# Kernel optimization log

Hardware: AMD Instinct MI355X
Metric: run time of the kernel (lower is better)

Reference implementation:

```python
import jax, jax.numpy as jnp
import numpy as np

N, T, D, H = 256, 128, 512, 1024


def setup_inputs() -> dict:
    key = jax.random.key(0)
    k_x, k_A, k_Wx, k_Wh, k_Wa = jax.random.split(key, 5)
    x = jax.random.normal(k_x, (N, T, D), dtype=jnp.float32)
    A = jax.random.normal(k_A, (N, H, 4, 4), dtype=jnp.float32)
    Wx = jax.random.normal(k_Wx, (D, 4 * H), dtype=jnp.float32) / np.sqrt(D)
    Wh = jax.random.normal(k_Wh, (H, 4 * H), dtype=jnp.float32) / np.sqrt(H)
    Wattn = jax.random.normal(k_Wa, (H, 4 * H), dtype=jnp.float32) / np.sqrt(H)
    b = jnp.zeros((4 * H,), dtype=jnp.float32)
    return {"x": x, "A": A, "Wx": Wx, "Wh": Wh, "Wattn": Wattn, "b": b}


def _attention_lstm(x, A, Wx, Wh, Wattn, b):
    # A: (N, H, 4, 4) -> flatten spatial to (N, H, 16)
    A_flat = A.reshape(A.shape[0], A.shape[1], -1)
    h0 = A_flat.mean(axis=2)  # (N, H)
    c0 = h0
    Hdim = h0.shape[1]
    scale = 1.0 / jnp.sqrt(jnp.asarray(Hdim, dtype=x.dtype))

    def step(carry, x_t):
        prev_h, prev_c = carry
        # scaled dot-product attention over 16 spatial locations
        scores = jnp.einsum("nh,nhs->ns", prev_h, A_flat) * scale  # (N, 16)
        w = jax.nn.softmax(scores, axis=1)
        attn = jnp.einsum("nhs,ns->nh", A_flat, w)  # (N, H)
        # fused LSTM gates
        a = x_t @ Wx + prev_h @ Wh + attn @ Wattn + b  # (N, 4H)
        i = jax.nn.sigmoid(a[:, 0:Hdim])
        f = jax.nn.sigmoid(a[:, Hdim:2 * Hdim])
        o = jax.nn.sigmoid(a[:, 2 * Hdim:3 * Hdim])
        g = jnp.tanh(a[:, 3 * Hdim:4 * Hdim])
        next_c = f * prev_c + i * g
        next_h = o * jnp.tanh(next_c)
        return (next_h, next_c), next_h

    x_tnd = jnp.swapaxes(x, 0, 1)  # (T, N, D)
    _, h_tnh = jax.lax.scan(step, (h0, c0), x_tnd)
    return jnp.swapaxes(h_tnh, 0, 1)  # (N, T, H)


def reference(x, A, Wx, Wh, Wattn, b):
    return _attention_lstm(x, A, Wx, Wh, Wattn, b)
```

## Files before the change

kernel.cpp:

```cpp
#include <hip/hip_runtime.h>
#include <math.h>

#define NB 256
#define TT 128
#define DD 512
#define HH 1024
#define KHX 1536
#define KFB 2560
#define BK 128
#define NBLK4 256

typedef _Float16 half_t;
typedef _Float16 half8 __attribute__((ext_vector_type(8)));
typedef _Float16 half4v __attribute__((ext_vector_type(4)));
typedef _Float16 half2v __attribute__((ext_vector_type(2)));
typedef float f32x4 __attribute__((ext_vector_type(4)));


__global__ __launch_bounds__(256) void k_trans(const float* __restrict__ src,
        half_t* __restrict__ dst, int kstride, int koff, int nkt) {
    __shared__ half_t tile[64][65];
    int bk = blockIdx.x % nkt;
    int bn = blockIdx.x / nkt;
    int k0 = bk * 64, n0 = bn * 64;
    #pragma unroll
    for (int i = 0; i < 16; ++i) {
        int idx = i * 256 + threadIdx.x;
        int r = idx >> 6, c = idx & 63;
        tile[c][r] = (half_t)src[(size_t)(k0 + r) * 4096 + n0 + c];
    }
    __syncthreads();
    #pragma unroll
    for (int i = 0; i < 16; ++i) {
        int idx = i * 256 + threadIdx.x;
        int r = idx >> 6, c = idx & 63;
        dst[(size_t)(n0 + r) * kstride + koff + k0 + c] = tile[r][c];
    }
}

__global__ __launch_bounds__(256) void k_convX(const float* __restrict__ x,
        half_t* __restrict__ x16) {
    size_t base = ((size_t)blockIdx.x * 256 + threadIdx.x) * 32;
    #pragma unroll
    for (int u = 0; u < 4; ++u) {
        float4 a = ((const float4*)(x + base))[2 * u];
        float4 c = ((const float4*)(x + base))[2 * u + 1];
        half8 p;
        p[0] = (half_t)a.x; p[1] = (half_t)a.y; p[2] = (half_t)a.z; p[3] = (half_t)a.w;
        p[4] = (half_t)c.x; p[5] = (half_t)c.y; p[6] = (half_t)c.z; p[7] = (half_t)c.w;
        ((half8*)(x16 + base))[u] = p;
    }
}

__global__ __launch_bounds__(256) void k_convA2(const float* __restrict__ A,
        half_t* __restrict__ A16, half_t* __restrict__ AsT,
        float* __restrict__ cbuf, half_t* __restrict__ h16) {
    int n = blockIdx.x, tid = threadIdx.x;
    #pragma unroll
    for (int r = 0; r < 4; ++r) {
        int h = tid + r * 256;
        const float4* ap = (const float4*)(A + ((size_t)n * HH + h) * 16);
        float4 v0 = ap[0], v1 = ap[1], v2 = ap[2], v3 = ap[3];
        float a[16];
        a[0]=v0.x; a[1]=v0.y; a[2] =v0.z; a[3] =v0.w;
        a[4]=v1.x; a[5]=v1.y; a[6] =v1.z; a[7] =v1.w;
        a[8]=v2.x; a[9]=v2.y; a[10]=v2.z; a[11]=v2.w;
        a[12]=v3.x; a[13]=v3.y; a[14]=v3.z; a[15]=v3.w;
        float hv = 0.f;
        #pragma unroll
        for (int s = 0; s < 16; ++s) hv += a[s];
        hv *= (1.f / 16.f);
        size_t ci = (size_t)n * HH + h;
        cbuf[ci] = hv;
        h16[ci] = (half_t)hv;
        half8 q0, q1;
        #pragma unroll
        for (int s = 0; s < 8; ++s) { q0[s] = (half_t)a[s]; q1[s] = (half_t)a[s + 8]; }
        *(half8*)(A16 + ci * 16) = q0;
        *(half8*)(A16 + ci * 16 + 8) = q1;
        #pragma unroll
        for (int s = 0; s < 16; ++s)
            AsT[(size_t)n * 16 * HH + (size_t)s * HH + h] = (half_t)a[s];
    }
}

__global__ __launch_bounds__(256) void k_initsc(const half_t* __restrict__ h16,
        const half_t* __restrict__ A16,
        float* __restrict__ sc0, float* __restrict__ sc1, float* __restrict__ sc2) {
    __shared__ float sred[4][16];
    int n = blockIdx.x, tid = threadIdx.x;
    float ps[16];
    #pragma unroll
    for (int s = 0; s < 16; ++s) ps[s] = 0.f;
    #pragma unroll
    for (int r = 0; r < 4; ++r) {
        int h = tid + r * 256;
        size_t ci = (size_t)n * HH + h;
        float hv = (float)h16[ci];
        const half8* ap = (const half8*)(A16 + ci * 16);
        half8 a0 = ap[0], a1 = ap[1];
        #pragma unroll
        for (int s = 0; s < 8; ++s) {
            ps[s]     += hv * (float)a0[s];
            ps[s + 8] += hv * (float)a1[s];
        }
    }
    #pragma unroll
    for (int off = 32; off; off >>= 1)
        #pragma unroll
        for (int s = 0; s < 16; ++s) ps[s] += __shfl_xor(ps[s], off, 64);
    int wave = tid >> 6;
    if ((tid & 63) == 0)
        #pragma unroll
        for (int s = 0; s < 16; ++s) sred[wave][s] = ps[s];
    __syncthreads();
    if (tid < 16)
        sc0[(size_t)n * 16 + tid] =
            sred[0][tid] + sred[1][tid] + sred[2][tid] + sred[3][tid];
    if (tid < 112) {
        int x = 1 + tid / 16, s = tid % 16;
        sc0[((size_t)x * 256 + n) * 16 + s] = 0.f;
    }
    if (tid < 128) {
        int x = tid / 16, s = tid % 16;
        sc1[((size_t)x * 256 + n) * 16 + s] = 0.f;
        sc2[((size_t)x * 256 + n) * 16 + s] = 0.f;
    }
}

__global__ __launch_bounds__(256) void k_gemm_G(const half_t* __restrict__ AsT,
        const half_t* __restrict__ WaT, half_t* __restrict__ G16) {
    __shared__ half_t sAs[16][BK + 8];
    __shared__ half_t sB[4][16][BK + 8];
    int bid = blockIdx.x;
    int n = bid >> 6, jt = bid & 63;
    int j0 = jt * 16;
    int tid = threadIdx.x, wv = tid >> 6, lane = tid & 63;
    f32x4 acc = {};
    int srB = tid >> 2, scB = (tid & 3) * 32;
    int gB = srB >> 4, jcB = srB & 15;
    for (int it = 0; it < HH / BK; ++it) {
        int k0 = it * BK;
        if (tid < 128) {
            int r = tid >> 3, c = (tid & 7) * 16;
            const uint4* sp = (const uint4*)(AsT + (size_t)n * 16 * HH + (size_t)r * HH + k0 + c);
            uint4 u0 = sp[0], u1 = sp[1];
            *(uint4*)&sAs[r][c] = u0;
            *(uint4*)&sAs[r][c + 8] = u1;
        }
        {
            const half_t* src = WaT + ((size_t)(gB * HH + j0 + jcB)) * HH + k0 + scB;
            uint4 u0 = ((const uint4*)src)[0];
            uint4 u1 = ((const uint4*)src)[1];
            uint4 u2 = ((const uint4*)src)[2];
            uint4 u3 = ((const uint4*)src)[3];
            *((uint4*)&sB[gB][jcB][scB])      = u0;
            *((uint4*)&sB[gB][jcB][scB + 8])  = u1;
            *((uint4*)&sB[gB][jcB][scB + 16]) = u2;
            *((uint4*)&sB[gB][jcB][scB + 24]) = u3;
        }
        __syncthreads();
        int row16 = lane & 15, kg = lane >> 4;
        #pragma unroll
        for (int kc = 0; kc < BK / 32; ++kc) {
            half8 bf = *(const half8*)&sB[wv][row16][kc * 32 + kg * 8];
            half8 af = *(const half8*)&sAs[row16][kc * 32 + kg * 8];
            acc = __builtin_amdgcn_mfma_f32_16x16x32_f16(af, bf, acc, 0, 0, 0);
        }
        __syncthreads();
    }
    int col = lane & 15, rbase = (lane >> 4) * 4;
    size_t jf = (size_t)wv * HH + j0 + col;
    half4v o;
    o[0] = (half_t)acc[0]; o[1] = (half_t)acc[1];
    o[2] = (half_t)acc[2]; o[3] = (half_t)acc[3];
    *(half4v*)(G16 + ((size_t)n * 4096 + jf) * 16 + rbase) = o;
}

__global__ __launch_bounds__(256) void k_gemm_XW(const half_t* __restrict__ x16,
        const half_t* __restrict__ WhxT, half_t* __restrict__ XW16) {
    __shared__ half_t sA[128][72];
    __shared__ half_t sB[64][72];
    int bid = blockIdx.x;
    int bm = bid & 255;
    int bj = bid >> 8;
    int row0 = bm * 128;
    int col0 = bj * 64;
    int tid = threadIdx.x, wv = tid >> 6, lane = tid & 63;
    int la = lane & 15, kg = lane >> 4;
    int mh = wv & 1, jh = wv >> 1;
    f32x4 acc[4][2] = {};
    int srA = tid >> 1, scA = (tid & 1) * 32;
    int srB = tid >> 2, scB = (tid & 3) * 16;
    for (int c = 0; c < 8; ++c) {
        {
            const uint4* sp = (const uint4*)(x16 + (size_t)(row0 + srA) * DD + c * 64 + scA);
            uint4 u0 = sp[0], u1 = sp[1];
            *(uint4*)&sA[srA][scA] = u0;
            *(uint4*)&sA[srA][scA + 8] = u1;
        }
        {
            const uint4* sp = (const uint4*)(WhxT + (size_t)(col0 + srB) * KHX + c * 64 + scB);
            *(uint4*)&sB[srB][scB] = sp[0];
        }
        __syncthreads();
        #pragma unroll
        for (int ks = 0; ks < 2; ++ks) {
            half8 b0 = *(const half8*)&sB[jh * 32 + la][ks * 32 + kg * 8];
            half8 b1 = *(const half8*)&sB[jh * 32 + 16 + la][ks * 32 + kg * 8];
            #pragma unroll
            for (int m = 0; m < 4; ++m) {
                half8 af = *(const half8*)&sA[mh * 64 + m * 16 + la][ks * 32 + kg * 8];
                acc[m][0] = __builtin_amdgcn_mfma_f32_16x16x32_f16(af, b0, acc[m][0], 0, 0, 0);
                acc[m][1] = __builtin_amdgcn_mfma_f32_16x16x32_f16(af, b1, acc[m][1], 0, 0, 0);
            }
        }
        __syncthreads();
    }
    __syncthreads();
    half_t (*Cl)[72] = sA;
    #pragma unroll
    for (int m = 0; m < 4; ++m)
        #pragma unroll
        for (int jt = 0; jt < 2; ++jt)
            #pragma unroll
            for (int q = 0; q < 4; ++q) {
                int rl = mh * 64 + m * 16 + kg * 4 + q;
                int cl = jh * 32 + jt * 16 + la;
                Cl[rl][cl] = (half_t)acc[m][jt][q];
            }
    __syncthreads();
    int g = col0 >> 10;
    #pragma unroll
    for (int i = 0; i < 4; ++i) {
        int idx = tid + i * 256;
        int rl = idx >> 3, grp = idx & 7;
        int R = row0 + rl;
        int t = R & 127, nn = R >> 7;
        int mh2 = nn >> 7, nl2 = nn & 127;
        int jb2 = ((col0 & 1023) >> 3) + grp;
        size_t dst = ((((size_t)t * 128 + jb2) * 2 + mh2) * 128 + nl2) * 32 + g * 8;
        *(half8*)(XW16 + dst) = *(const half8*)&Cl[rl][grp * 8];
    }
}


struct StepLds4 {
    half_t W[32][1028];
    union {
        half_t H[128][260];
        float sm[4][128][16];
        struct {
            float pe[128][33];
            float pad[896];
            float ps[2][128][18];
        } e;
    } u;
};

__device__ __forceinline__ void grid_sync4(int* cnt, volatile int* flag, int inst) {
    __syncthreads();
    if (threadIdx.x == 0) {
        __threadfence();
        int prev = __hip_atomic_fetch_add(cnt, 1, __ATOMIC_RELAXED,
                                          __HIP_MEMORY_SCOPE_AGENT);
        if (prev == NBLK4 * (inst + 1) - 1) {
            __hip_atomic_store((int*)flag, inst + 1, __ATOMIC_RELAXED,
                               __HIP_MEMORY_SCOPE_AGENT);
        } else {
            int guard = 0;
            while (__hip_atomic_load((int*)flag, __ATOMIC_RELAXED,
                                     __HIP_MEMORY_SCOPE_AGENT) < inst + 1) {
                __builtin_amdgcn_s_sleep(2);
                if (++guard > (1 << 24)) break;
            }
        }
        __threadfence();
    }
    __syncthreads();
}

__global__ __launch_bounds__(512, 1) void k_steps4(
        const half_t* __restrict__ XW16, half_t* __restrict__ h16A,
        half_t* __restrict__ h16B, const half_t* __restrict__ WhxT,
        const half_t* __restrict__ A16, const half_t* __restrict__ G16,
        const float* __restrict__ b, const float* __restrict__ cbuf,
        float* __restrict__ sc0, float* __restrict__ sc1, float* __restrict__ sc2,
        float* __restrict__ out, int* __restrict__ bar) {
    __shared__ StepLds4 L;
    int bid = blockIdx.x;
    int mhalf = bid & 1, jb = bid >> 1;
    int n0 = mhalf * 128;
    int tid = threadIdx.x;
    int wv = tid >> 6, lane = tid & 63;
    int la = lane & 15, kg = lane >> 4;
    int srow = tid >> 2, sseg = tid & 3;
    int slice = bid & 7;
    int* cnt = bar;
    volatile int* flag = (volatile int*)(bar + 32);

    {
        int wr = tid >> 4, seg = tid & 15;
        const half_t* wsrc = WhxT + (size_t)((wr >> 3) * HH + jb * 8 + (wr & 7)) * KHX
                           + DD + seg * 64;
        #pragma unroll
        for (int i = 0; i < 8; ++i)
            *(uint4*)&L.W[wr][seg * 64 + i * 8] = ((const uint4*)wsrc)[i];
    }

    int n_l = tid & 127, jg2 = tid >> 7;
    int n = n0 + n_l;
    int jbase = jb * 8 + jg2 * 2;
    half8 gq[4][4];
    #pragma unroll
    for (int g = 0; g < 4; ++g) {
        const half8* gsrc = (const half8*)(G16 + ((size_t)n * 4096 + g * HH + jbase) * 16);
        #pragma unroll
        for (int i = 0; i < 4; ++i) gq[g][i] = gsrc[i];
    }
    half8 aq[4];
    {
        const half8* asrc = (const half8*)(A16 + ((size_t)n * HH + jbase) * 16);
        #pragma unroll
        for (int i = 0; i < 4; ++i) aq[i] = asrc[i];
    }
    float bb[4][2];
    #pragma unroll
    for (int g = 0; g < 4; ++g) {
        bb[g][0] = b[g * HH + jbase];
        bb[g][1] = b[g * HH + jbase + 1];
    }
    float creg[2];
    creg[0] = cbuf[(size_t)n * HH + jbase];
    creg[1] = cbuf[(size_t)n * HH + jbase + 1];

    float* scC = sc0; float* scN = sc1; float* scZ = sc2;
    half_t* h16c = h16A;
    half_t* h16n = h16B;

    half2v xwv[4];
    {
        const half_t* xwp = XW16 + (((size_t)jb * 2 + mhalf) * 128 + n_l) * 32;
        #pragma unroll
        for (int g = 0; g < 4; ++g) xwv[g] = *(const half2v*)(xwp + g * 8 + jg2 * 2);
    }

    for (int t = 0; t < TT; ++t) {
        if (bid < 64) ((float*)scZ)[bid * 512 + tid] = 0.f;

        {
            const float* p0 = scC + ((size_t)(jg2 * 2) * 256 + n) * 16;
            const float* p1 = scC + ((size_t)(jg2 * 2 + 1) * 256 + n) * 16;
            #pragma unroll
            for (int i = 0; i < 4; ++i) {
                float4 a = ((const float4*)p0)[i];
                float4 c = ((const float4*)p1)[i];
                float4 o;
                o.x = a.x + c.x; o.y = a.y + c.y; o.z = a.z + c.z; o.w = a.w + c.w;
                *(float4*)&L.u.sm[jg2][n_l][4 * i] = o;
            }
        }
        __syncthreads();
        float w16[16];
        {
            float sc[16];
            #pragma unroll
            for (int i = 0; i < 4; ++i) {
                float4 q0 = *(const float4*)&L.u.sm[0][n_l][4 * i];
                float4 q1 = *(const float4*)&L.u.sm[1][n_l][4 * i];
                float4 q2 = *(const float4*)&L.u.sm[2][n_l][4 * i];
                float4 q3 = *(const float4*)&L.u.sm[3][n_l][4 * i];
                sc[4 * i + 0] = q0.x + q1.x + q2.x + q3.x;
                sc[4 * i + 1] = q0.y + q1.y + q2.y + q3.y;
                sc[4 * i + 2] = q0.z + q1.z + q2.z + q3.z;
                sc[4 * i + 3] = q0.w + q1.w + q2.w + q3.w;
            }
            float m = -1e30f;
            #pragma unroll
            for (int s = 0; s < 16; ++s) { sc[s] *= 0.03125f; m = fmaxf(m, sc[s]); }
            float den = 0.f;
            #pragma unroll
            for (int s = 0; s < 16; ++s) { sc[s] = expf(sc[s] - m); den += sc[s]; }
            float inv = 1.f / den;
            #pragma unroll
            for (int s = 0; s < 16; ++s) w16[s] = sc[s] * inv;
        }

        f32x4 acc0 = {}, acc1 = {};
        uint4 r[8];
        {
            const half_t* src = h16c + (size_t)(n0 + srow) * HH + sseg * 64;
            #pragma unroll
            for (int i = 0; i < 8; ++i) r[i] = ((const uint4*)src)[i];
        }
        __syncthreads();
        #pragma unroll 1
        for (int c = 0; c < 4; ++c) {
            #pragma unroll
            for (int i = 0; i < 8; ++i)
                *(uint4*)&L.u.H[srow][sseg * 64 + i * 8] = r[i];
            __syncthreads();
            if (c + 1 < 4) {
                const half_t* src = h16c + (size_t)(n0 + srow) * HH + (c + 1) * 256 + sseg * 64;
                #pragma unroll
                for (int i = 0; i < 8; ++i) r[i] = ((const uint4*)src)[i];
            }
            #pragma unroll
            for (int ks = 0; ks < 8; ++ks) {
                half8 af = *(const half8*)&L.u.H[wv * 16 + la][ks * 32 + kg * 8];
                half8 b0 = *(const half8*)&L.W[la][c * 256 + ks * 32 + kg * 8];
                half8 b1 = *(const half8*)&L.W[16 + la][c * 256 + ks * 32 + kg * 8];
                acc0 = __builtin_amdgcn_mfma_f32_16x16x32_f16(af, b0, acc0, 0, 0, 0);
                acc1 = __builtin_amdgcn_mfma_f32_16x16x32_f16(af, b1, acc1, 0, 0, 0);
            }
            __syncthreads();
        }

        #pragma unroll
        for (int q = 0; q < 4; ++q) {
            L.u.e.pe[wv * 16 + kg * 4 + q][la]      = acc0[q];
            L.u.e.pe[wv * 16 + kg * 4 + q][16 + la] = acc1[q];
        }
        __syncthreads();

        float v[4][2];
        #pragma unroll
        for (int g = 0; g < 4; ++g) {
            #pragma unroll
            for (int jj = 0; jj < 2; ++jj) {
                float a0 = 0.f;
                #pragma unroll
                for (int s = 0; s < 16; ++s)
                    a0 += w16[s] * (float)gq[g][jj * 2 + (s >> 3)][s & 7];
                v[g][jj] = L.u.e.pe[n_l][g * 8 + jg2 * 2 + jj] + bb[g][jj]
                         + (float)xwv[g][jj] + a0;
            }
        }
        float hv[2];
        #pragma unroll
        for (int jj = 0; jj < 2; ++jj) {
            float ig = 1.f / (1.f + expf(-v[0][jj]));
            float fg = 1.f / (1.f + expf(-v[1][jj]));
            float og = 1.f / (1.f + expf(-v[2][jj]));
            float gg = tanhf(v[3][jj]);
            float cn = fg * creg[jj] + ig * gg;
            creg[jj] = cn;
            hv[jj] = og * tanhf(cn);
        }
        {
            float2 o2; o2.x = hv[0]; o2.y = hv[1];
            *(float2*)(out + ((size_t)n * TT + t) * HH + jbase) = o2;
            half2v h2; h2[0] = (half_t)hv[0]; h2[1] = (half_t)hv[1];
            *(half2v*)(h16n + (size_t)n * HH + jbase) = h2;
        }
        float p[16];
        #pragma unroll
        for (int s = 0; s < 16; ++s)
            p[s] = hv[0] * (float)aq[s >> 3][s & 7]
                 + hv[1] * (float)aq[2 + (s >> 3)][s & 7];
        int pair = jg2 >> 1;
        if ((jg2 & 1) == 0) {
            #pragma unroll
            for (int s = 0; s < 16; ++s) L.u.e.ps[pair][n_l][s] = p[s];
        }
        __syncthreads();
        if ((jg2 & 1) == 1) {
            #pragma unroll
            for (int s = 0; s < 16; ++s) L.u.e.ps[pair][n_l][s] += p[s];
        }
        __syncthreads();
        #pragma unroll
        for (int i = 0; i < 4; ++i) {
            int slot = tid * 4 + i;
            int nn = slot >> 4, s = slot & 15;
            atomicAdd(scN + ((size_t)slice * 256 + n0 + nn) * 16 + s,
                      L.u.e.ps[0][nn][s] + L.u.e.ps[1][nn][s]);
        }

        if (t + 1 < TT) {
            half2v xwn[4];
            const half_t* xwp = XW16 + ((((size_t)(t + 1) * 128 + jb) * 2 + mhalf) * 128 + n_l) * 32;
            #pragma unroll
            for (int g = 0; g < 4; ++g) xwn[g] = *(const half2v*)(xwp + g * 8 + jg2 * 2);
            grid_sync4(cnt, flag, t);
            #pragma unroll
            for (int g = 0; g < 4; ++g) xwv[g] = xwn[g];
        }
        float* tmp = scC; scC = scN; scN = scZ; scZ = tmp;
        half_t* th = h16c; h16c = h16n; h16n = th;
    }
}


__global__ __launch_bounds__(256) void k_convA(const float* __restrict__ A,
        half_t* __restrict__ A16, half_t* __restrict__ AsT,
        float* __restrict__ cbuf, half_t* __restrict__ h16,
        float* __restrict__ sc0, float* __restrict__ sc1, float* __restrict__ sc2) {
    __shared__ float sred[4][16];
    int n = blockIdx.x, tid = threadIdx.x;
    float ps[16];
    #pragma unroll
    for (int s = 0; s < 16; ++s) ps[s] = 0.f;
    #pragma unroll
    for (int r = 0; r < 4; ++r) {
        int h = tid + r * 256;
        const float4* ap = (const float4*)(A + ((size_t)n * HH + h) * 16);
        float4 v0 = ap[0], v1 = ap[1], v2 = ap[2], v3 = ap[3];
        float a[16];
        a[0]=v0.x; a[1]=v0.y; a[2] =v0.z; a[3] =v0.w;
        a[4]=v1.x; a[5]=v1.y; a[6] =v1.z; a[7] =v1.w;
        a[8]=v2.x; a[9]=v2.y; a[10]=v2.z; a[11]=v2.w;
        a[12]=v3.x; a[13]=v3.y; a[14]=v3.z; a[15]=v3.w;
        float hv = 0.f;
        #pragma unroll
        for (int s = 0; s < 16; ++s) hv += a[s];
        hv *= (1.f / 16.f);
        size_t ci = (size_t)n * HH + h;
        cbuf[ci] = hv;
        h16[ci] = (half_t)hv;
        half8 q0, q1;
        #pragma unroll
        for (int s = 0; s < 8; ++s) { q0[s] = (half_t)a[s]; q1[s] = (half_t)a[s + 8]; }
        *(half8*)(A16 + ci * 16) = q0;
        *(half8*)(A16 + ci * 16 + 8) = q1;
        #pragma unroll
        for (int s = 0; s < 16; ++s)
            AsT[(size_t)n * 16 * HH + (size_t)s * HH + h] = (half_t)a[s];
        #pragma unroll
        for (int s = 0; s < 16; ++s) ps[s] += hv * a[s];
    }
    #pragma unroll
    for (int off = 32; off; off >>= 1)
        #pragma unroll
        for (int s = 0; s < 16; ++s) ps[s] += __shfl_xor(ps[s], off, 64);
    int wave = tid >> 6;
    if ((tid & 63) == 0)
        #pragma unroll
        for (int s = 0; s < 16; ++s) sred[wave][s] = ps[s];
    __syncthreads();
    if (tid < 16) {
        sc0[n * 16 + tid] = sred[0][tid] + sred[1][tid] + sred[2][tid] + sred[3][tid];
        sc1[n * 16 + tid] = 0.f;
        sc2[n * 16 + tid] = 0.f;
    }
}

union LdsS {
    struct {
        half_t sA[32][BK + 8];
        half_t sB[4][16][BK + 8];
    } s;
    float pe[4][32][16];
};

__global__ __launch_bounds__(256) void k_step(const float* __restrict__ x,
        const half_t* __restrict__ h16c, half_t* __restrict__ h16n,
        const half_t* __restrict__ WhxT, const half_t* __restrict__ A16,
        const half_t* __restrict__ G16, const float* __restrict__ b,
        float* __restrict__ cbuf, const float* __restrict__ scC,
        float* __restrict__ scN, float* __restrict__ scZ,
        float* __restrict__ out, int t) {
    __shared__ LdsS L;
    __shared__ float wlds[32][16];
    int bid = blockIdx.x;
    int xcd = bid & 7, slot = bid >> 3;
    int mtile = slot & 7, jtile = slot >> 3;
    int n0 = mtile * 32;
    int j0 = xcd * 128 + jtile * 16;
    int tid = threadIdx.x, wv = tid >> 6, lane = tid & 63;

    if (bid < 16) scZ[bid * 256 + tid] = 0.f;
    if (tid < 32) {
        int n = n0 + tid;
        const float4* sp = (const float4*)(scC + n * 16);
        float4 u0 = sp[0], u1 = sp[1], u2 = sp[2], u3 = sp[3];
        float sc[16] = {u0.x, u0.y, u0.z, u0.w, u1.x, u1.y, u1.z, u1.w,
                        u2.x, u2.y, u2.z, u2.w, u3.x, u3.y, u3.z, u3.w};
        float m = -1e30f;
        #pragma unroll
        for (int s = 0; s < 16; ++s) { sc[s] *= 0.03125f; m = fmaxf(m, sc[s]); }
        float den = 0.f;
        #pragma unroll
        for (int s = 0; s < 16; ++s) { sc[s] = expf(sc[s] - m); den += sc[s]; }
        float inv = 1.f / den;
        #pragma unroll
        for (int s = 0; s < 16; ++s) wlds[tid][s] = sc[s] * inv;
    }

    f32x4 acc[2] = {};
    int srA = tid >> 3, scA = (tid & 7) * 16;
    int srB = tid >> 2, scB = (tid & 3) * 32;
    int gB = srB >> 4, jcB = srB & 15;

    for (int it = 0; it < KHX / BK; ++it) {
        int k0 = it * BK;
        {
            int n = n0 + srA;
            if (k0 < DD) {
                const float* src = x + ((size_t)n * TT + t) * DD + k0 + scA;
                float4 v0 = ((const float4*)src)[0];
                float4 v1 = ((const float4*)src)[1];
                float4 v2 = ((const float4*)src)[2];
                float4 v3 = ((const float4*)src)[3];
                half8 p0, p1;
                p0[0] = (half_t)v0.x; p0[1] = (half_t)v0.y; p0[2] = (half_t)v0.z; p0[3] = (half_t)v0.w;
                p0[4] = (half_t)v1.x; p0[5] = (half_t)v1.y; p0[6] = (half_t)v1.z; p0[7] = (half_t)v1.w;
                p1[0] = (half_t)v2.x; p1[1] = (half_t)v2.y; p1[2] = (half_t)v2.z; p1[3] = (half_t)v2.w;
                p1[4] = (half_t)v3.x; p1[5] = (half_t)v3.y; p1[6] = (half_t)v3.z; p1[7] = (half_t)v3.w;
                *(half8*)&L.s.sA[srA][scA]     = p0;
                *(half8*)&L.s.sA[srA][scA + 8] = p1;
            } else {
                const half_t* srch = h16c + (size_t)n * HH + (k0 - DD) + scA;
                uint4 u0 = ((const uint4*)srch)[0];
                uint4 u1 = ((const uint4*)srch)[1];
                *((uint4*)&L.s.sA[srA][scA])     = u0;
                *((uint4*)&L.s.sA[srA][scA + 8]) = u1;
            }
        }
        {
            const half_t* src = WhxT + ((size_t)(gB * HH + j0 + jcB)) * KHX + k0 + scB;
            uint4 u0 = ((const uint4*)src)[0];
            uint4 u1 = ((const uint4*)src)[1];
            uint4 u2 = ((const uint4*)src)[2];
            uint4 u3 = ((const uint4*)src)[3];
            *((uint4*)&L.s.sB[gB][jcB][scB])      = u0;
            *((uint4*)&L.s.sB[gB][jcB][scB + 8])  = u1;
            *((uint4*)&L.s.sB[gB][jcB][scB + 16]) = u2;
            *((uint4*)&L.s.sB[gB][jcB][scB + 24]) = u3;
        }
        __syncthreads();
        int row16 = lane & 15, kg = lane >> 4;
        #pragma unroll
        for (int kc = 0; kc < BK / 32; ++kc) {
            half8 bf = *(const half8*)&L.s.sB[wv][row16][kc * 32 + kg * 8];
            #pragma unroll
            for (int m = 0; m < 2; ++m) {
                half8 af = *(const half8*)&L.s.sA[row16 + m * 16][kc * 32 + kg * 8];
                acc[m] = __builtin_amdgcn_mfma_f32_16x16x32_f16(af, bf, acc[m], 0, 0, 0);
            }
        }
        __syncthreads();
    }
    {
        int col = lane & 15, rbase = (lane >> 4) * 4;
        #pragma unroll
        for (int m = 0; m < 2; ++m)
            #pragma unroll
            for (int q = 0; q < 4; ++q)
                L.pe[wv][m * 16 + rbase + q][col] = acc[m][q];
    }
    __syncthreads();
    #pragma unroll
    for (int q2 = 0; q2 < 2; ++q2) {
        int idx = tid + q2 * 256;
        int r = idx >> 4, jc = idx & 15;
        int n = n0 + r, j = j0 + jc;
        float wv16[16];
        #pragma unroll
        for (int s = 0; s < 16; ++s) wv16[s] = wlds[r][s];
        float v[4];
        v[0] = L.pe[0][r][jc] + b[j];
        v[1] = L.pe[1][r][jc] + b[HH + j];
        v[2] = L.pe[2][r][jc] + b[2 * HH + j];
        v[3] = L.pe[3][r][jc] + b[3 * HH + j];
        #pragma unroll
        for (int g = 0; g < 4; ++g) {
            const half8* gq = (const half8*)(G16 + ((size_t)n * 4096 + g * HH + j) * 16);
            half8 ga = gq[0], gb2 = gq[1];
            float a0 = 0.f;
            #pragma unroll
            for (int s = 0; s < 8; ++s)
                a0 += wv16[s] * (float)ga[s] + wv16[s + 8] * (float)gb2[s];
            v[g] += a0;
        }
        float ig = 1.f / (1.f + expf(-v[0]));
        float fg = 1.f / (1.f + expf(-v[1]));
        float og = 1.f / (1.f + expf(-v[2]));
        float gg = tanhf(v[3]);
        size_t ci = (size_t)n * HH + j;
        float cp = cbuf[ci];
        float cn = fg * cp + ig * gg;
        cbuf[ci] = cn;
        float hv = og * tanhf(cn);
        out[((size_t)n * TT + t) * HH + j] = hv;
        h16n[ci] = (half_t)hv;
        const half8* ap = (const half8*)(A16 + ci * 16);
        half8 a0 = ap[0], a1 = ap[1];
        float p[16];
        #pragma unroll
        for (int s = 0; s < 8; ++s) { p[s] = hv * (float)a0[s]; p[s + 8] = hv * (float)a1[s]; }
        #pragma unroll
        for (int msk = 1; msk < 16; msk <<= 1)
            #pragma unroll
            for (int s = 0; s < 16; ++s) p[s] += __shfl_xor(p[s], msk, 64);
        float myp = 0.f;
        #pragma unroll
        for (int s = 0; s < 16; ++s) myp = (jc == s) ? p[s] : myp;
        atomicAdd(scN + n * 16 + jc, myp);
    }
}


__global__ __launch_bounds__(256) void fb_wconv(const float* __restrict__ Wx,
        const float* __restrict__ Wh, const float* __restrict__ Wa,
        half_t* __restrict__ WT) {
    __shared__ half_t tile[64][65];
    int bk = blockIdx.x % 40;
    int bn = blockIdx.x / 40;
    int k0 = bk * 64, n0 = bn * 64;
    #pragma unroll
    for (int i = 0; i < 16; ++i) {
        int idx = i * 256 + threadIdx.x;
        int r = idx >> 6, c = idx & 63;
        int k = k0 + r, n = n0 + c;
        float v;
        if (k < DD)            v = Wx[(size_t)k * 4096 + n];
        else if (k < DD + HH)  v = Wh[(size_t)(k - DD) * 4096 + n];
        else                   v = Wa[(size_t)(k - DD - HH) * 4096 + n];
        tile[c][r] = (half_t)v;
    }
    __syncthreads();
    #pragma unroll
    for (int i = 0; i < 16; ++i) {
        int idx = i * 256 + threadIdx.x;
        int r = idx >> 6, c = idx & 63;
        WT[(size_t)(n0 + r) * KFB + k0 + c] = tile[r][c];
    }
}

__global__ __launch_bounds__(256) void fb_init(const float* __restrict__ A,
        float* __restrict__ h0, float* __restrict__ c0) {
    int n = blockIdx.x;
    #pragma unroll
    for (int r = 0; r < 4; ++r) {
        int h = threadIdx.x + r * 256;
        const float4* ap = (const float4*)(A + ((size_t)n * HH + h) * 16);
        float s = 0.f;
        #pragma unroll
        for (int q = 0; q < 4; ++q) {
            float4 v = ap[q];
            s += v.x + v.y + v.z + v.w;
        }
        s *= (1.f / 16.f);
        h0[n * HH + h] = s;
        c0[n * HH + h] = s;
    }
}

__global__ __launch_bounds__(256) void fb_attn(const float* __restrict__ A,
        const float* __restrict__ hprev, long long hstride,
        half_t* __restrict__ h16, half_t* __restrict__ attn16) {
    __shared__ float sh[HH];
    __shared__ float sred[4][16];
    int n = blockIdx.x;
    const float* hp = hprev + (size_t)n * hstride;
    #pragma unroll
    for (int r = 0; r < 4; ++r) {
        int h = threadIdx.x + r * 256;
        float v = hp[h];
        sh[h] = v;
        h16[n * HH + h] = (half_t)v;
    }
    __syncthreads();
    float a[4][16];
    float ps[16];
    #pragma unroll
    for (int s = 0; s < 16; ++s) ps[s] = 0.f;
    #pragma unroll
    for (int r = 0; r < 4; ++r) {
        int h = threadIdx.x + r * 256;
        const float4* ap = (const float4*)(A + ((size_t)n * HH + h) * 16);
        float4 v0 = ap[0], v1 = ap[1], v2 = ap[2], v3 = ap[3];
        a[r][0] = v0.x;  a[r][1] = v0.y;  a[r][2]  = v0.z;  a[r][3]  = v0.w;
        a[r][4] = v1.x;  a[r][5] = v1.y;  a[r][6]  = v1.z;  a[r][7]  = v1.w;
        a[r][8] = v2.x;  a[r][9] = v2.y;  a[r][10] = v2.z;  a[r][11] = v2.w;
        a[r][12] = v3.x; a[r][13] = v3.y; a[r][14] = v3.z;  a[r][15] = v3.w;
        float hh = sh[h];
        #pragma unroll
        for (int s = 0; s < 16; ++s) ps[s] += hh * a[r][s];
    }
    #pragma unroll
    for (int off = 32; off; off >>= 1)
        #pragma unroll
        for (int s = 0; s < 16; ++s) ps[s] += __shfl_xor(ps[s], off, 64);
    int wave = threadIdx.x >> 6;
    if ((threadIdx.x & 63) == 0)
        #pragma unroll
        for (int s = 0; s < 16; ++s) sred[wave][s] = ps[s];
    __syncthreads();
    float sc[16], m = -1e30f;
    #pragma unroll
    for (int s = 0; s < 16; ++s) {
        sc[s] = (sred[0][s] + sred[1][s] + sred[2][s] + sred[3][s]) * 0.03125f;
        m = fmaxf(m, sc[s]);
    }
    float den = 0.f;
    #pragma unroll
    for (int s = 0; s < 16; ++s) { sc[s] = expf(sc[s] - m); den += sc[s]; }
    float inv = 1.f / den;
    #pragma unroll
    for (int r = 0; r < 4; ++r) {
        int h = threadIdx.x + r * 256;
        float acc = 0.f;
        #pragma unroll
        for (int s = 0; s < 16; ++s) acc += a[r][s] * sc[s];
        attn16[n * HH + h] = (half_t)(acc * inv);
    }
}

union LdsFB {
    struct {
        half_t sA[32][BK + 8];
        half_t sB[4][16][BK + 8];
    } s;
    float pe[4][32][16];
};

__global__ __launch_bounds__(256) void fb_gemm(const float* __restrict__ x,
        const half_t* __restrict__ h16, const half_t* __restrict__ attn16,
        const half_t* __restrict__ WT, const float* __restrict__ b,
        float* __restrict__ cbuf, float* __restrict__ out, int t) {
    __shared__ LdsFB L;
    int bid = blockIdx.x;
    int xcd = bid & 7;
    int slot = bid >> 3;
    int mtile = slot & 7;
    int jtile = slot >> 3;
    int m0 = mtile * 32;
    int j0 = xcd * 128 + jtile * 16;
    int tid = threadIdx.x;
    int wv = tid >> 6, lane = tid & 63;
    f32x4 acc[2] = {};
    int srA = tid >> 3, scA = (tid & 7) * 16;
    int srB = tid >> 2, scB = (tid & 3) * 32;
    int gB = srB >> 4, jcB = srB & 15;
    for (int it = 0; it < KFB / BK; ++it) {
        int k0 = it * BK;
        {
            int n = m0 + srA;
            if (k0 < DD) {
                const float* src = x + ((size_t)n * TT + t) * DD + k0 + scA;
                float4 v0 = ((const float4*)src)[0];
                float4 v1 = ((const float4*)src)[1];
                float4 v2 = ((const float4*)src)[2];
                float4 v3 = ((const float4*)src)[3];
                half8 p0, p1;
                p0[0] = (half_t)v0.x; p0[1] = (half_t)v0.y; p0[2] = (half_t)v0.z; p0[3] = (half_t)v0.w;
                p0[4] = (half_t)v1.x; p0[5] = (half_t)v1.y; p0[6] = (half_t)v1.z; p0[7] = (half_t)v1.w;
                p1[0] = (half_t)v2.x; p1[1] = (half_t)v2.y; p1[2] = (half_t)v2.z; p1[3] = (half_t)v2.w;
                p1[4] = (half_t)v3.x; p1[5] = (half_t)v3.y; p1[6] = (half_t)v3.z; p1[7] = (half_t)v3.w;
                *(half8*)&L.s.sA[srA][scA]     = p0;
                *(half8*)&L.s.sA[srA][scA + 8] = p1;
            } else {
                const half_t* srch = (k0 < DD + HH)
                    ? (h16    + (size_t)n * HH + (k0 - DD)      + scA)
                    : (attn16 + (size_t)n * HH + (k0 - DD - HH) + scA);
                uint4 u0 = ((const uint4*)srch)[0];
                uint4 u1 = ((const uint4*)srch)[1];
                *((uint4*)&L.s.sA[srA][scA])     = u0;
                *((uint4*)&L.s.sA[srA][scA + 8]) = u1;
            }
        }
        {
            const half_t* src = WT + ((size_t)(gB * HH + j0 + jcB)) * KFB + k0 + scB;
            uint4 u0 = ((const uint4*)src)[0];
            uint4 u1 = ((const uint4*)src)[1];
            uint4 u2 = ((const uint4*)src)[2];
            uint4 u3 = ((const uint4*)src)[3];
            *((uint4*)&L.s.sB[gB][jcB][scB])      = u0;
            *((uint4*)&L.s.sB[gB][jcB][scB + 8])  = u1;
            *((uint4*)&L.s.sB[gB][jcB][scB + 16]) = u2;
            *((uint4*)&L.s.sB[gB][jcB][scB + 24]) = u3;
        }
        __syncthreads();
        int row16 = lane & 15, kg = lane >> 4;
        #pragma unroll
        for (int kc = 0; kc < BK / 32; ++kc) {
            half8 bf = *(const half8*)&L.s.sB[wv][row16][kc * 32 + kg * 8];
            #pragma unroll
            for (int m = 0; m < 2; ++m) {
                half8 af = *(const half8*)&L.s.sA[row16 + m * 16][kc * 32 + kg * 8];
                acc[m] = __builtin_amdgcn_mfma_f32_16x16x32_f16(af, bf, acc[m], 0, 0, 0);
            }
        }
        __syncthreads();
    }
    {
        int col = lane & 15, rbase = (lane >> 4) * 4;
        #pragma unroll
        for (int m = 0; m < 2; ++m)
            #pragma unroll
            for (int q = 0; q < 4; ++q)
                L.pe[wv][m * 16 + rbase + q][col] = acc[m][q];
    }
    __syncthreads();
    #pragma unroll
    for (int q2 = 0; q2 < 2; ++q2) {
        int idx = tid + q2 * 256;
        int r = idx >> 4, jc = idx & 15;
        int n = m0 + r, j = j0 + jc;
        float vi = L.pe[0][r][jc] + b[j];
        float vf = L.pe[1][r][jc] + b[HH + j];
        float vo = L.pe[2][r][jc] + b[2 * HH + j];
        float vg = L.pe[3][r][jc] + b[3 * HH + j];
        float ig = 1.f / (1.f + expf(-vi));
        float fg = 1.f / (1.f + expf(-vf));
        float og = 1.f / (1.f + expf(-vo));
        float gg = tanhf(vg);
        size_t ci = (size_t)n * HH + j;
        float cp = cbuf[ci];
        float cn = fg * cp + ig * gg;
        cbuf[ci] = cn;
        out[((size_t)n * TT + t) * HH + j] = og * tanhf(cn);
    }
}


extern "C" void kernel_launch(void* const* d_in, const int* in_sizes, int n_in,
                              void* d_out, int out_size, void* d_ws, size_t ws_size,
                              hipStream_t stream) {
    const float* x  = (const float*)d_in[0];
    const float* A  = (const float*)d_in[1];
    const float* Wx = (const float*)d_in[2];
    const float* Wh = (const float*)d_in[3];
    const float* Wa = (const float*)d_in[4];
    const float* b  = (const float*)d_in[5];
    float* out = (float*)d_out;
    char* ws = (char*)d_ws;

    int maxb = 0;
    hipError_t oe = hipOccupancyMaxActiveBlocksPerMultiprocessor(&maxb, k_steps4, 512, 0);
    bool persistent_ok = (oe == hipSuccess && maxb >= 1);

    if (ws_size >= 375439616ULL && persistent_ok) {
        half_t* WhxT = (half_t*)(ws);
        half_t* WaT  = (half_t*)(ws + 12582912);
        half_t* A16  = (half_t*)(ws + 20971520);
        half_t* AsT  = (half_t*)(ws + 29360128);
        half_t* G16  = (half_t*)(ws + 37748736);
        half_t* h16a = (half_t*)(ws + 71303168);
        half_t* h16b = (half_t*)(ws + 71827456);
        float*  cb   = (float*) (ws + 72351744);
        half_t* x16  = (half_t*)(ws + 73449472);
        int*    bar  = (int*)   (ws + 107003904);
        half_t* XW16 = (half_t*)(ws + 107004160);
        float*  sc0  = (float*)(ws + 29360128);
        float*  sc1  = (float*)(ws + 29360128 + 32768);
        float*  sc2  = (float*)(ws + 29360128 + 65536);

        hipLaunchKernelGGL(k_trans, dim3(8 * 64),  dim3(256), 0, stream, Wx, WhxT, KHX, 0,   8);
        hipLaunchKernelGGL(k_trans, dim3(16 * 64), dim3(256), 0, stream, Wh, WhxT, KHX, 512, 16);
        hipLaunchKernelGGL(k_trans, dim3(16 * 64), dim3(256), 0, stream, Wa, WaT,  HH,  0,   16);
        hipLaunchKernelGGL(k_convX, dim3(2048), dim3(256), 0, stream, x, x16);
        hipLaunchKernelGGL(k_convA2, dim3(256), dim3(256), 0, stream, A, A16, AsT, cb, h16a);
        hipLaunchKernelGGL(k_gemm_G, dim3(NB * 64), dim3(256), 0, stream, AsT, WaT, G16);
        hipLaunchKernelGGL(k_gemm_XW, dim3(256 * 64), dim3(256), 0, stream, x16, WhxT, XW16);
        hipLaunchKernelGGL(k_initsc, dim3(256), dim3(256), 0, stream, h16a, A16, sc0, sc1, sc2);
        hipMemsetAsync(bar, 0, 256, stream);
        hipLaunchKernelGGL(k_steps4, dim3(NBLK4), dim3(512), 0, stream,
                           XW16, h16a, h16b, WhxT, A16, G16, b, cb,
                           sc0, sc1, sc2, out, bar);
    } else if (ws_size >= 73449472ULL) {
        half_t* WhxT = (half_t*)(ws);
        half_t* WaT  = (half_t*)(ws + 12582912);
        half_t* A16  = (half_t*)(ws + 20971520);
        half_t* AsT  = (half_t*)(ws + 29360128);
        half_t* G16  = (half_t*)(ws + 37748736);
        half_t* h16a = (half_t*)(ws + 71303168);
        half_t* h16b = (half_t*)(ws + 71827456);
        float*  cb   = (float*) (ws + 72351744);
        float*  sc0  = (float*) (ws + 73400320);
        float*  sc1  = (float*) (ws + 73416704);
        float*  sc2  = (float*) (ws + 73433088);
        float* scb[3] = {sc0, sc1, sc2};

        hipLaunchKernelGGL(k_trans, dim3(8 * 64),  dim3(256), 0, stream, Wx, WhxT, KHX, 0,   8);
        hipLaunchKernelGGL(k_trans, dim3(16 * 64), dim3(256), 0, stream, Wh, WhxT, KHX, 512, 16);
        hipLaunchKernelGGL(k_trans, dim3(16 * 64), dim3(256), 0, stream, Wa, WaT,  HH,  0,   16);
        hipLaunchKernelGGL(k_convA, dim3(256), dim3(256), 0, stream,
                           A, A16, AsT, cb, h16a, sc0, sc1, sc2);
        hipLaunchKernelGGL(k_gemm_G, dim3(NB * 64), dim3(256), 0, stream, AsT, WaT, G16);
        for (int t = 0; t < TT; ++t) {
            float* scC = scb[t % 3];
            float* scN = scb[(t + 1) % 3];
            float* scZ = scb[(t + 2) % 3];
            half_t* h16c = (t & 1) ? h16b : h16a;
            half_t* h16n = (t & 1) ? h16a : h16b;
            hipLaunchKernelGGL(k_step, dim3(512), dim3(256), 0, stream,
                               x, h16c, h16n, WhxT, A16, G16, b, cb, scC, scN, scZ, out, t);
        }
    } else {
        half_t* WT  = (half_t*)ws;
        float*  h0  = (float*)(ws + 20971520);
        float*  cb  = (float*)(ws + 22020096);
        half_t* h16 = (half_t*)(ws + 23068672);
        half_t* a16 = (half_t*)(ws + 23592960);
        hipLaunchKernelGGL(fb_wconv, dim3(2560), dim3(256), 0, stream, Wx, Wh, Wa, WT);
        hipLaunchKernelGGL(fb_init, dim3(256), dim3(256), 0, stream, A, h0, cb);
        for (int t = 0; t < TT; ++t) {
            const float* hp = (t == 0) ? h0 : (out + (size_t)(t - 1) * HH);
            long long hstride = (t == 0) ? (long long)HH : (long long)TT * HH;
            hipLaunchKernelGGL(fb_attn, dim3(256), dim3(256), 0, stream, A, hp, hstride, h16, a16);
            hipLaunchKernelGGL(fb_gemm, dim3(512), dim3(256), 0, stream,
                               x, h16, a16, WT, b, cb, out, t);
        }
    }
}
```

Measured before the change: 4.641 ms.

## Split grid barrier per batch half and read h directly from global in MFMA loop

```diff
diff --git a/kernel.cpp b/kernel.cpp
--- a/kernel.cpp
+++ b/kernel.cpp
@@ -8,7 +8,8 @@
 #define KHX 1536
 #define KFB 2560
 #define BK 128
-#define NBLK4 256
+#define NBLK5 256
+#define NHALF 128
 
 typedef _Float16 half_t;
 typedef _Float16 half8 __attribute__((ext_vector_type(8)));
@@ -245,31 +246,30 @@
 }
 
 
-struct StepLds4 {
+struct StepLds5 {
     half_t W[32][1028];
     union {
-        half_t H[128][260];
         float sm[4][128][16];
         struct {
             float pe[128][33];
-            float pad[896];
+            float pad[384];
             float ps[2][128][18];
         } e;
     } u;
 };
 
-__device__ __forceinline__ void grid_sync4(int* cnt, volatile int* flag, int inst) {
+__device__ __forceinline__ void grid_sync5(int* cnt, int* flag, int inst) {
     __syncthreads();
     if (threadIdx.x == 0) {
         __threadfence();
         int prev = __hip_atomic_fetch_add(cnt, 1, __ATOMIC_RELAXED,
                                           __HIP_MEMORY_SCOPE_AGENT);
-        if (prev == NBLK4 * (inst + 1) - 1) {
-            __hip_atomic_store((int*)flag, inst + 1, __ATOMIC_RELAXED,
+        if (prev == NHALF * (inst + 1) - 1) {
+            __hip_atomic_store(flag, inst + 1, __ATOMIC_RELAXED,
                                __HIP_MEMORY_SCOPE_AGENT);
         } else {
             int guard = 0;
-            while (__hip_atomic_load((int*)flag, __ATOMIC_RELAXED,
+            while (__hip_atomic_load(flag, __ATOMIC_RELAXED,
                                      __HIP_MEMORY_SCOPE_AGENT) < inst + 1) {
                 __builtin_amdgcn_s_sleep(2);
                 if (++guard > (1 << 24)) break;
@@ -280,24 +280,23 @@
     __syncthreads();
 }
 
-__global__ __launch_bounds__(512, 1) void k_steps4(
+__global__ __launch_bounds__(512, 1) void k_steps5(
         const half_t* __restrict__ XW16, half_t* __restrict__ h16A,
         half_t* __restrict__ h16B, const half_t* __restrict__ WhxT,
         const half_t* __restrict__ A16, const half_t* __restrict__ G16,
         const float* __restrict__ b, const float* __restrict__ cbuf,
         float* __restrict__ sc0, float* __restrict__ sc1, float* __restrict__ sc2,
         float* __restrict__ out, int* __restrict__ bar) {
-    __shared__ StepLds4 L;
+    __shared__ StepLds5 L;
     int bid = blockIdx.x;
     int mhalf = bid & 1, jb = bid >> 1;
     int n0 = mhalf * 128;
     int tid = threadIdx.x;
     int wv = tid >> 6, lane = tid & 63;
     int la = lane & 15, kg = lane >> 4;
-    int srow = tid >> 2, sseg = tid & 3;
     int slice = bid & 7;
-    int* cnt = bar;
-    volatile int* flag = (volatile int*)(bar + 32);
+    int* cnt  = bar + mhalf * 32;
+    int* flag = bar + mhalf * 32 + 16;
 
     {
         int wr = tid >> 4, seg = tid & 15;
@@ -346,7 +345,12 @@
     }
 
     for (int t = 0; t < TT; ++t) {
-        if (bid < 64) ((float*)scZ)[bid * 512 + tid] = 0.f;
+        if (jb < 32) {
+            int idx = jb * 512 + tid;
+            int sl = idx >> 11, rem = idx & 2047;
+            int nn = rem >> 4, s = rem & 15;
+            scZ[((size_t)sl * 256 + n0 + nn) * 16 + s] = 0.f;
+        }
 
         {
             const float* p0 = scC + ((size_t)(jg2 * 2) * 256 + n) * 16;
@@ -385,35 +389,19 @@
             #pragma unroll
             for (int s = 0; s < 16; ++s) w16[s] = sc[s] * inv;
         }
+        __syncthreads();
 
         f32x4 acc0 = {}, acc1 = {};
-        uint4 r[8];
-        {
-            const half_t* src = h16c + (size_t)(n0 + srow) * HH + sseg * 64;
-            #pragma unroll
-            for (int i = 0; i < 8; ++i) r[i] = ((const uint4*)src)[i];
-        }
-        __syncthreads();
-        #pragma unroll 1
-        for (int c = 0; c < 4; ++c) {
-            #pragma unroll
-            for (int i = 0; i < 8; ++i)
-                *(uint4*)&L.u.H[srow][sseg * 64 + i * 8] = r[i];
-            __syncthreads();
-            if (c + 1 < 4) {
-                const half_t* src = h16c + (size_t)(n0 + srow) * HH + (c + 1) * 256 + sseg * 64;
-                #pragma unroll
-                for (int i = 0; i < 8; ++i) r[i] = ((const uint4*)src)[i];
-            }
-            #pragma unroll
-            for (int ks = 0; ks < 8; ++ks) {
-                half8 af = *(const half8*)&L.u.H[wv * 16 + la][ks * 32 + kg * 8];
-                half8 b0 = *(const half8*)&L.W[la][c * 256 + ks * 32 + kg * 8];
-                half8 b1 = *(const half8*)&L.W[16 + la][c * 256 + ks * 32 + kg * 8];
+        {
+            const half_t* hrow = h16c + (size_t)(n0 + wv * 16 + la) * HH + kg * 8;
+            #pragma unroll
+            for (int c = 0; c < 32; ++c) {
+                half8 af = *(const half8*)(hrow + c * 32);
+                half8 b0 = *(const half8*)&L.W[la][c * 32 + kg * 8];
+                half8 b1 = *(const half8*)&L.W[16 + la][c * 32 + kg * 8];
                 acc0 = __builtin_amdgcn_mfma_f32_16x16x32_f16(af, b0, acc0, 0, 0, 0);
                 acc1 = __builtin_amdgcn_mfma_f32_16x16x32_f16(af, b1, acc1, 0, 0, 0);
             }
-            __syncthreads();
         }
 
         #pragma unroll
@@ -482,7 +470,7 @@
             const half_t* xwp = XW16 + ((((size_t)(t + 1) * 128 + jb) * 2 + mhalf) * 128 + n_l) * 32;
             #pragma unroll
             for (int g = 0; g < 4; ++g) xwn[g] = *(const half2v*)(xwp + g * 8 + jg2 * 2);
-            grid_sync4(cnt, flag, t);
+            grid_sync5(cnt, flag, t);
             #pragma unroll
             for (int g = 0; g < 4; ++g) xwv[g] = xwn[g];
         }
@@ -929,7 +917,7 @@
     char* ws = (char*)d_ws;
 
     int maxb = 0;
-    hipError_t oe = hipOccupancyMaxActiveBlocksPerMultiprocessor(&maxb, k_steps4, 512, 0);
+    hipError_t oe = hipOccupancyMaxActiveBlocksPerMultiprocessor(&maxb, k_steps5, 512, 0);
     bool persistent_ok = (oe == hipSuccess && maxb >= 1);
 
     if (ws_size >= 375439616ULL && persistent_ok) {
@@ -957,7 +945,7 @@
         hipLaunchKernelGGL(k_gemm_XW, dim3(256 * 64), dim3(256), 0, stream, x16, WhxT, XW16);
         hipLaunchKernelGGL(k_initsc, dim3(256), dim3(256), 0, stream, h16a, A16, sc0, sc1, sc2);
         hipMemsetAsync(bar, 0, 256, stream);
-        hipLaunchKernelGGL(k_steps4, dim3(NBLK4), dim3(512), 0, stream,
+        hipLaunchKernelGGL(k_steps5, dim3(NBLK5), dim3(512), 0, stream,
                            XW16, h16a, h16b, WhxT, A16, G16, b, cb,
                            sc0, sc1, sc2, out, bar);
     } else if (ws_size >= 73449472ULL) {
```

After: 4.626 ms. About the same (-0.3%).
